# Performance work log

Measured on AMD Instinct MI355X. Metric: run time of the kernel, lower is better.

The kernel has to match this reference:

```python
import jax, jax.numpy as jnp
import numpy as np

B, S, D = 4, 2048, 512
H = 8
DEPTH = D // H  # 64


def setup_inputs() -> dict:
    key = jax.random.key(0)
    ks = jax.random.split(key, 6)
    scale = 1.0 / np.sqrt(D)
    return {
        "x": jax.random.normal(ks[0], (B, S, D), dtype=jnp.float32),
        "y": jax.random.normal(ks[1], (B, S, D), dtype=jnp.float32),
        "W_q": jax.random.normal(ks[2], (D, D), dtype=jnp.float32) * scale,
        "W_k": jax.random.normal(ks[3], (D, D), dtype=jnp.float32) * scale,
        "W_v": jax.random.normal(ks[4], (D, D), dtype=jnp.float32) * scale,
        "W_o": jax.random.normal(ks[5], (D, D), dtype=jnp.float32) * scale,
    }


def _split_heads(t):
    # [B, S, D] -> [B, H, S, DEPTH]
    b, s, _ = t.shape
    return t.reshape(b, s, H, DEPTH).transpose(0, 2, 1, 3)


def reference(x, y, W_q, W_k, W_v, W_o):
    q = _split_heads(x @ W_q) * (DEPTH ** -0.5)   # [B,H,Sq,d]
    k = _split_heads(y @ W_k)                      # [B,H,Sk,d]
    v = _split_heads(y @ W_v)                      # [B,H,Sk,d]
    logits = jnp.einsum("bhqd,bhkd->bhqk", q, k)   # [B,H,Sq,Sk]
    weights = jax.nn.softmax(logits, axis=-1)
    attn = jnp.einsum("bhqk,bhkd->bhqd", weights, v)  # [B,H,Sq,d]
    attn = attn.transpose(0, 2, 1, 3).reshape(x.shape[0], x.shape[1], D)
    return attn @ W_o
```

## Files before the change

### kernel.cpp

```cpp
#include <hip/hip_runtime.h>
#include <hip/hip_bf16.h>
#include <math.h>
#include <stdint.h>

#define NB 4
#define NS 2048
#define ND 512
#define NH 8
#define DEP 64

typedef __attribute__((ext_vector_type(8))) short bf16x8;
typedef __attribute__((ext_vector_type(4))) short bf16x4;
typedef __attribute__((ext_vector_type(4))) float f32x4;
typedef __attribute__((ext_vector_type(16))) float f32x16;

#define QSCALE 0.18033688011112042f

__device__ __forceinline__ short f2b(float f) {
  unsigned u = __float_as_uint(f);
  u += 0x7FFF + ((u >> 16) & 1);
  return (short)(u >> 16);
}
__device__ __forceinline__ unsigned pk2(float a, float b) {
  union { __hip_bfloat162 h; unsigned u; } c;
  c.h = __float22bfloat162_rn(float2{a, b});
  return c.u;
}
__device__ __forceinline__ void dma16(const void* g, void* l) {
  __builtin_amdgcn_global_load_lds(
      (const __attribute__((address_space(1))) void*)g,
      (__attribute__((address_space(3))) void*)l, 16, 0, 0);
}

__global__ __launch_bounds__(256) void prep(
    const float* __restrict__ x, const float* __restrict__ y,
    const float* __restrict__ W0, const float* __restrict__ W1,
    const float* __restrict__ W2, const float* __restrict__ W3,
    short* __restrict__ xb, short* __restrict__ yb, short* __restrict__ T0,
    short* __restrict__ T1, short* __restrict__ T2, short* __restrict__ T3) {
  const int t = threadIdx.x;
  if (blockIdx.y < 2) {
    const float* src = blockIdx.y ? y : x;
    short* dst = blockIdx.y ? yb : xb;
    size_t i = ((size_t)blockIdx.x * 256 + t) * 4;
    float4 v = *(const float4*)(src + i);
    bf16x4 o;
    o[0] = f2b(v.x); o[1] = f2b(v.y); o[2] = f2b(v.z); o[3] = f2b(v.w);
    *(bf16x4*)(dst + i) = o;
    return;
  }
  const int bx = blockIdx.x;
  if (bx >= 256) return;
  const int wj = bx >> 6, rem = bx & 63;
  const float* W = wj == 0 ? W0 : wj == 1 ? W1 : wj == 2 ? W2 : W3;
  short* T = wj == 0 ? T0 : wj == 1 ? T1 : wj == 2 ? T2 : T3;
  __shared__ float tile[64][65];
  const int k0 = (rem >> 3) * 64, n0 = (rem & 7) * 64;
#pragma unroll
  for (int i = 0; i < 4; ++i) {
    int r = (t >> 4) + i * 16;
    int c = (t & 15) * 4;
    float4 v = *(const float4*)&W[(size_t)(k0 + r) * ND + n0 + c];
    tile[r][c] = v.x; tile[r][c + 1] = v.y;
    tile[r][c + 2] = v.z; tile[r][c + 3] = v.w;
  }
  __syncthreads();
#pragma unroll
  for (int i = 0; i < 4; ++i) {
    int n = (t >> 4) + i * 16;
    int kc = (t & 15) * 4;
    bf16x4 o;
#pragma unroll
    for (int j = 0; j < 4; ++j) o[j] = f2b(tile[kc + j][n]);
    *(bf16x4*)&T[(size_t)(n0 + n) * ND + k0 + kc] = o;
  }
}

__device__ __forceinline__ void gemm128(const short* __restrict__ A,
                                        const short* __restrict__ Bt,
                                        short* __restrict__ Cout, int mode,
                                        float alpha) {
  __shared__ short As[128 * 64];
  __shared__ short Bs[128 * 64];
  const int t = threadIdx.x;
  const int wave = t >> 6, lane = t & 63;
  const int m = lane & 15, quad = lane >> 4;
  const int m0 = blockIdx.y * 128, n0 = blockIdx.x * 128;
  const int mh = (wave >> 1) * 64, nh = (wave & 1) * 64;
  const int r8 = lane >> 3;
  const int c8 = (lane & 7) ^ r8;
  const int mx7 = m & 7;
  f32x4 acc[4][4];
#pragma unroll
  for (int i = 0; i < 4; ++i)
#pragma unroll
    for (int j = 0; j < 4; ++j) acc[i][j] = (f32x4){0.f, 0.f, 0.f, 0.f};

  for (int k0 = 0; k0 < ND; k0 += 64) {
    __syncthreads();
#pragma unroll
    for (int i = 0; i < 4; ++i) {
      int row = i * 32 + wave * 8 + r8;
      dma16(A + (size_t)(m0 + row) * ND + k0 + c8 * 8,
            As + (i * 256 + wave * 64) * 8);
      dma16(Bt + (size_t)(n0 + row) * ND + k0 + c8 * 8,
            Bs + (i * 256 + wave * 64) * 8);
    }
    __syncthreads();
    bf16x8 af[4][2], bf[4][2];
#pragma unroll
    for (int mt = 0; mt < 4; ++mt)
#pragma unroll
      for (int kc = 0; kc < 2; ++kc)
        af[mt][kc] = *(const bf16x8*)(As + (mh + mt * 16 + m) * 64 +
                                      ((kc * 4 + quad) ^ mx7) * 8);
#pragma unroll
    for (int nt = 0; nt < 4; ++nt)
#pragma unroll
      for (int kc = 0; kc < 2; ++kc)
        bf[nt][kc] = *(const bf16x8*)(Bs + (nh + nt * 16 + m) * 64 +
                                      ((kc * 4 + quad) ^ mx7) * 8);
#pragma unroll
    for (int mt = 0; mt < 4; ++mt)
#pragma unroll
      for (int nt = 0; nt < 4; ++nt)
#pragma unroll
        for (int kc = 0; kc < 2; ++kc)
          acc[mt][nt] = __builtin_amdgcn_mfma_f32_16x16x32_bf16(
              af[mt][kc], bf[nt][kc], acc[mt][nt], 0, 0, 0);
  }
  if (mode == 2) {
#pragma unroll
    for (int mt = 0; mt < 4; ++mt)
#pragma unroll
      for (int nt = 0; nt < 4; ++nt) {
        int row0 = m0 + mh + mt * 16 + quad * 4;
        int col = n0 + nh + nt * 16 + m;
        int b_ = row0 >> 11, s_ = row0 & (NS - 1);
        int h_ = col >> 6, d_ = col & (DEP - 1);
        uint2 p;
        p.x = pk2(acc[mt][nt][0] * alpha, acc[mt][nt][1] * alpha);
        p.y = pk2(acc[mt][nt][2] * alpha, acc[mt][nt][3] * alpha);
        *(uint2*)(Cout + (size_t)((b_ * NH + h_) * DEP + d_) * NS + s_) = p;
      }
  } else {
#pragma unroll
    for (int mt = 0; mt < 4; ++mt)
#pragma unroll
      for (int nt = 0; nt < 4; ++nt)
#pragma unroll
        for (int r = 0; r < 4; ++r) {
          int row = m0 + mh + mt * 16 + quad * 4 + r;
          int col = n0 + nh + nt * 16 + m;
          Cout[(size_t)row * ND + col] = f2b(acc[mt][nt][r] * alpha);
        }
  }
}

__global__ __launch_bounds__(256) void qkv_gemm(
    const short* __restrict__ xb, const short* __restrict__ yb,
    const short* __restrict__ Wqt, const short* __restrict__ Wkt,
    const short* __restrict__ Wvt, short* __restrict__ Qb,
    short* __restrict__ Kb, short* __restrict__ Vtb) {
  if (blockIdx.z == 0)
    gemm128(xb, Wqt, Qb, 1, QSCALE);
  else if (blockIdx.z == 1)
    gemm128(yb, Wkt, Kb, 1, 1.0f);
  else
    gemm128(yb, Wvt, Vtb, 2, 1.0f);
}

__global__ __launch_bounds__(256) void out_gemm(const short* __restrict__ A,
                                                const short* __restrict__ Bt,
                                                float* __restrict__ Cout) {
  __shared__ short As[2][128 * 64];
  __shared__ short Bs[2][64 * 64];
  const int t = threadIdx.x;
  const int wave = t >> 6, lane = t & 63;
  const int m = lane & 15, quad = lane >> 4;
  const int m0 = blockIdx.y * 128, n0 = blockIdx.x * 64;
  const int mh = (wave >> 1) * 64, nh = (wave & 1) * 32;
  const int r8 = lane >> 3;
  const int c8 = (lane & 7) ^ r8;
  const int mx7 = m & 7;
  f32x4 acc[4][2];
#pragma unroll
  for (int i = 0; i < 4; ++i)
#pragma unroll
    for (int j = 0; j < 2; ++j) acc[i][j] = (f32x4){0.f, 0.f, 0.f, 0.f};

#pragma unroll
  for (int i = 0; i < 4; ++i)
    dma16(A + (size_t)(m0 + i * 32 + wave * 8 + r8) * ND + c8 * 8,
          As[0] + (i * 256 + wave * 64) * 8);
#pragma unroll
  for (int i = 0; i < 2; ++i)
    dma16(Bt + (size_t)(n0 + i * 32 + wave * 8 + r8) * ND + c8 * 8,
          Bs[0] + (i * 256 + wave * 64) * 8);

  int buf = 0;
  for (int k0 = 0; k0 < ND; k0 += 64, buf ^= 1) {
    __syncthreads();
    if (k0 + 64 < ND) {
#pragma unroll
      for (int i = 0; i < 4; ++i)
        dma16(A + (size_t)(m0 + i * 32 + wave * 8 + r8) * ND + k0 + 64 + c8 * 8,
              As[buf ^ 1] + (i * 256 + wave * 64) * 8);
#pragma unroll
      for (int i = 0; i < 2; ++i)
        dma16(Bt + (size_t)(n0 + i * 32 + wave * 8 + r8) * ND + k0 + 64 +
                  c8 * 8,
              Bs[buf ^ 1] + (i * 256 + wave * 64) * 8);
    }
    bf16x8 af[4][2], bf[2][2];
#pragma unroll
    for (int mt = 0; mt < 4; ++mt)
#pragma unroll
      for (int kc = 0; kc < 2; ++kc)
        af[mt][kc] = *(const bf16x8*)(As[buf] + (mh + mt * 16 + m) * 64 +
                                      ((kc * 4 + quad) ^ mx7) * 8);
#pragma unroll
    for (int nt = 0; nt < 2; ++nt)
#pragma unroll
      for (int kc = 0; kc < 2; ++kc)
        bf[nt][kc] = *(const bf16x8*)(Bs[buf] + (nh + nt * 16 + m) * 64 +
                                      ((kc * 4 + quad) ^ mx7) * 8);
#pragma unroll
    for (int mt = 0; mt < 4; ++mt)
#pragma unroll
      for (int nt = 0; nt < 2; ++nt)
#pragma unroll
        for (int kc = 0; kc < 2; ++kc)
          acc[mt][nt] = __builtin_amdgcn_mfma_f32_16x16x32_bf16(
              af[mt][kc], bf[nt][kc], acc[mt][nt], 0, 0, 0);
  }
#pragma unroll
  for (int mt = 0; mt < 4; ++mt)
#pragma unroll
    for (int nt = 0; nt < 2; ++nt)
#pragma unroll
      for (int r = 0; r < 4; ++r) {
        int row = m0 + mh + mt * 16 + quad * 4 + r;
        int col = n0 + nh + nt * 16 + m;
        Cout[(size_t)row * ND + col] = acc[mt][nt][r];
      }
}

__global__ __launch_bounds__(256) void attn_mfma(const short* __restrict__ Qb,
                                                 const short* __restrict__ Kb,
                                                 const short* __restrict__ Vtb,
                                                 short* __restrict__ Ob) {
  __shared__ short Ks[2][64 * 64];
  __shared__ short Vts[2][64 * 64];
  const int t = threadIdx.x;
  const int wave = t >> 6, lane = t & 63;
  const int l31 = lane & 31, hi = lane >> 5;
  const int sw = lane & 7;
  const int bh = blockIdx.y, b = bh >> 3, h = bh & 7;
  const int q0 = blockIdx.x * 128 + wave * 32;
  const size_t rowb = (size_t)b * NS;
  const short* Vtbase = Vtb + (size_t)(bh * DEP) * NS;
  const int r8 = lane >> 3;
  const int c8 = (lane & 7) ^ r8;

  bf16x8 qf[4];
#pragma unroll
  for (int dc = 0; dc < 4; ++dc)
    qf[dc] = *(const bf16x8*)(Qb + (rowb + q0 + l31) * ND + h * DEP + dc * 16 +
                              hi * 8);

  float l_ = 0.0f;
  f32x16 Ot[2];
#pragma unroll
  for (int dt = 0; dt < 2; ++dt)
#pragma unroll
    for (int i = 0; i < 16; ++i) Ot[dt][i] = 0.f;

#pragma unroll
  for (int i = 0; i < 2; ++i) {
    int row = i * 32 + wave * 8 + r8;
    dma16(Kb + (rowb + row) * ND + h * DEP + c8 * 8,
          Ks[0] + (i * 256 + wave * 64) * 8);
    dma16(Vtbase + (size_t)row * NS + c8 * 8,
          Vts[0] + (i * 256 + wave * 64) * 8);
  }

  int buf = 0;
  for (int kv0 = 0; kv0 < NS; kv0 += 64, buf ^= 1) {
    __syncthreads();
    if (kv0 + 64 < NS) {
#pragma unroll
      for (int i = 0; i < 2; ++i) {
        int row = i * 32 + wave * 8 + r8;
        dma16(Kb + (rowb + kv0 + 64 + row) * ND + h * DEP + c8 * 8,
              Ks[buf ^ 1] + (i * 256 + wave * 64) * 8);
        dma16(Vtbase + (size_t)row * NS + kv0 + 64 + c8 * 8,
              Vts[buf ^ 1] + (i * 256 + wave * 64) * 8);
      }
    }

    f32x16 St[2];
#pragma unroll
    for (int kt = 0; kt < 2; ++kt)
#pragma unroll
      for (int i = 0; i < 16; ++i) St[kt][i] = 0.f;
#pragma unroll
    for (int kt = 0; kt < 2; ++kt)
#pragma unroll
      for (int dc = 0; dc < 4; ++dc) {
        bf16x8 kf = *(const bf16x8*)(&Ks[buf][(kt * 32 + l31) * 64 +
                                              ((dc * 2 + hi) ^ sw) * 8]);
        St[kt] = __builtin_amdgcn_mfma_f32_32x32x16_bf16(kf, qf[dc], St[kt],
                                                         0, 0, 0);
      }

    bf16x8 pf[4];
    float rs = 0.f;
#pragma unroll
    for (int s = 0; s < 4; ++s) {
      const int kt = s >> 1, base = (s & 1) * 8;
      float E[8];
#pragma unroll
      for (int j = 0; j < 8; ++j) {
        E[j] = __builtin_amdgcn_exp2f(St[kt][base + j]);
        rs += E[j];
      }
      unsigned A0 = pk2(E[0], E[1]), A1 = pk2(E[2], E[3]);
      unsigned A2 = pk2(E[4], E[5]), A3 = pk2(E[6], E[7]);
      auto r02 =
          __builtin_amdgcn_permlane32_swap((int)A0, (int)A2, false, false);
      auto r13 =
          __builtin_amdgcn_permlane32_swap((int)A1, (int)A3, false, false);
      union { bf16x8 v; int u[4]; } pu;
      pu.u[0] = r02[0]; pu.u[1] = r13[0]; pu.u[2] = r02[1]; pu.u[3] = r13[1];
      pf[s] = pu.v;
    }
    l_ += rs;

#pragma unroll
    for (int dt = 0; dt < 2; ++dt)
#pragma unroll
      for (int s = 0; s < 4; ++s) {
        bf16x8 vf = *(const bf16x8*)(&Vts[buf][(dt * 32 + l31) * 64 +
                                               ((s * 2 + hi) ^ sw) * 8]);
        Ot[dt] = __builtin_amdgcn_mfma_f32_32x32x16_bf16(vf, pf[s], Ot[dt],
                                                         0, 0, 0);
      }
  }

  l_ += __shfl_xor(l_, 32, 64);
  float linv = 1.0f / l_;
  size_t row = rowb + q0 + l31;
#pragma unroll
  for (int dt = 0; dt < 2; ++dt)
#pragma unroll
    for (int g = 0; g < 4; ++g) {
      uint2 pk;
      pk.x = pk2(Ot[dt][g * 4 + 0] * linv, Ot[dt][g * 4 + 1] * linv);
      pk.y = pk2(Ot[dt][g * 4 + 2] * linv, Ot[dt][g * 4 + 3] * linv);
      *(uint2*)(Ob + row * ND + h * DEP + dt * 32 + g * 8 + hi * 4) = pk;
    }
}

extern "C" void kernel_launch(void* const* d_in, const int* in_sizes, int n_in,
                              void* d_out, int out_size, void* d_ws,
                              size_t ws_size, hipStream_t stream) {
  const float* x = (const float*)d_in[0];
  const float* y = (const float*)d_in[1];
  const float* Wq = (const float*)d_in[2];
  const float* Wk = (const float*)d_in[3];
  const float* Wv = (const float*)d_in[4];
  const float* Wo = (const float*)d_in[5];
  float* out = (float*)d_out;

  const size_t mat = (size_t)NB * NS * ND;
  const size_t wsz = (size_t)ND * ND;
  short* xb = (short*)d_ws;
  short* yb = xb + mat;
  short* Wqt = yb + mat;
  short* Wkt = Wqt + wsz;
  short* Wvt = Wkt + wsz;
  short* Wot = Wvt + wsz;
  short* Qb = Wot + wsz;
  short* Kb = Qb + mat;
  short* Vtb = Kb + mat;
  short* attnb = xb;

  prep<<<dim3(mat / 1024, 3), 256, 0, stream>>>(x, y, Wq, Wk, Wv, Wo, xb, yb,
                                                Wqt, Wkt, Wvt, Wot);
  qkv_gemm<<<dim3(ND / 128, (NB * NS) / 128, 3), 256, 0, stream>>>(
      xb, yb, Wqt, Wkt, Wvt, Qb, Kb, Vtb);
  attn_mfma<<<dim3(NS / 128, NB * NH), 256, 0, stream>>>(Qb, Kb, Vtb, attnb);
  out_gemm<<<dim3(ND / 64, (NB * NS) / 128), 256, 0, stream>>>(attnb, Wot,
                                                               out);
}
```

Before: 190.1 us.

## Split attention KV range across two wave groups and merge partials in LDS

The attention kernel now launches 512 threads per block. Two groups of four waves each process half of the key/value sequence for the same 128 queries. The second group writes its unnormalized output and row sums to shared memory, and the first group adds them in, normalizes, and stores the result. This doubles the waves available per block to hide latency, since the grid has only 512 blocks. The cost is double the LDS footprint, an extra merge step with barriers, and more register pressure under the launch-bounds hint. It also makes a small change to the first QK MFMA, which now starts from a zero accumulator, and to the row-sum reduction order.

Result: faster. 184.3 us (-3.1%).

```diff
diff --git a/kernel.cpp b/kernel.cpp
--- a/kernel.cpp
+++ b/kernel.cpp
@@ -8,6 +8,7 @@
 #define ND 512
 #define NH 8
 #define DEP 64
+#define KVHALF (NS / 2)
 
 typedef __attribute__((ext_vector_type(8))) short bf16x8;
 typedef __attribute__((ext_vector_type(4))) short bf16x4;
@@ -246,18 +247,19 @@
       }
 }
 
-__global__ __launch_bounds__(256) void attn_mfma(const short* __restrict__ Qb,
-                                                 const short* __restrict__ Kb,
-                                                 const short* __restrict__ Vtb,
-                                                 short* __restrict__ Ob) {
-  __shared__ short Ks[2][64 * 64];
-  __shared__ short Vts[2][64 * 64];
+__global__ __launch_bounds__(512, 4) void attn_mfma(
+    const short* __restrict__ Qb, const short* __restrict__ Kb,
+    const short* __restrict__ Vtb, short* __restrict__ Ob) {
+  __shared__ short Ks[2][2][64 * 64];
+  __shared__ short Vts[2][2][64 * 64];
   const int t = threadIdx.x;
   const int wave = t >> 6, lane = t & 63;
+  const int zh = wave >> 2, wl = wave & 3;
   const int l31 = lane & 31, hi = lane >> 5;
   const int sw = lane & 7;
   const int bh = blockIdx.y, b = bh >> 3, h = bh & 7;
-  const int q0 = blockIdx.x * 128 + wave * 32;
+  const int q0 = blockIdx.x * 128 + wl * 32;
+  const int kvb = zh * KVHALF;
   const size_t rowb = (size_t)b * NS;
   const short* Vtbase = Vtb + (size_t)(bh * DEP) * NS;
   const int r8 = lane >> 3;
@@ -269,6 +271,10 @@
     qf[dc] = *(const bf16x8*)(Qb + (rowb + q0 + l31) * ND + h * DEP + dc * 16 +
                               hi * 8);
 
+  f32x16 kzero;
+#pragma unroll
+  for (int i = 0; i < 16; ++i) kzero[i] = 0.f;
+
   float l_ = 0.0f;
   f32x16 Ot[2];
 #pragma unroll
@@ -278,41 +284,42 @@
 
 #pragma unroll
   for (int i = 0; i < 2; ++i) {
-    int row = i * 32 + wave * 8 + r8;
-    dma16(Kb + (rowb + row) * ND + h * DEP + c8 * 8,
-          Ks[0] + (i * 256 + wave * 64) * 8);
-    dma16(Vtbase + (size_t)row * NS + c8 * 8,
-          Vts[0] + (i * 256 + wave * 64) * 8);
+    int row = i * 32 + wl * 8 + r8;
+    dma16(Kb + (rowb + kvb + row) * ND + h * DEP + c8 * 8,
+          &Ks[zh][0][(i * 256 + wl * 64) * 8]);
+    dma16(Vtbase + (size_t)row * NS + kvb + c8 * 8,
+          &Vts[zh][0][(i * 256 + wl * 64) * 8]);
   }
 
   int buf = 0;
-  for (int kv0 = 0; kv0 < NS; kv0 += 64, buf ^= 1) {
+  for (int kv0 = 0; kv0 < KVHALF; kv0 += 64, buf ^= 1) {
     __syncthreads();
-    if (kv0 + 64 < NS) {
+    if (kv0 + 64 < KVHALF) {
 #pragma unroll
       for (int i = 0; i < 2; ++i) {
-        int row = i * 32 + wave * 8 + r8;
-        dma16(Kb + (rowb + kv0 + 64 + row) * ND + h * DEP + c8 * 8,
-              Ks[buf ^ 1] + (i * 256 + wave * 64) * 8);
-        dma16(Vtbase + (size_t)row * NS + kv0 + 64 + c8 * 8,
-              Vts[buf ^ 1] + (i * 256 + wave * 64) * 8);
+        int row = i * 32 + wl * 8 + r8;
+        dma16(Kb + (rowb + kvb + kv0 + 64 + row) * ND + h * DEP + c8 * 8,
+              &Ks[zh][buf ^ 1][(i * 256 + wl * 64) * 8]);
+        dma16(Vtbase + (size_t)row * NS + kvb + kv0 + 64 + c8 * 8,
+              &Vts[zh][buf ^ 1][(i * 256 + wl * 64) * 8]);
       }
     }
 
     f32x16 St[2];
 #pragma unroll
-    for (int kt = 0; kt < 2; ++kt)
-#pragma unroll
-      for (int i = 0; i < 16; ++i) St[kt][i] = 0.f;
-#pragma unroll
-    for (int kt = 0; kt < 2; ++kt)
-#pragma unroll
-      for (int dc = 0; dc < 4; ++dc) {
-        bf16x8 kf = *(const bf16x8*)(&Ks[buf][(kt * 32 + l31) * 64 +
-                                              ((dc * 2 + hi) ^ sw) * 8]);
+    for (int kt = 0; kt < 2; ++kt) {
+      bf16x8 kf0 = *(const bf16x8*)(&Ks[zh][buf][(kt * 32 + l31) * 64 +
+                                                 (hi ^ sw) * 8]);
+      St[kt] = __builtin_amdgcn_mfma_f32_32x32x16_bf16(kf0, qf[0], kzero,
+                                                       0, 0, 0);
+#pragma unroll
+      for (int dc = 1; dc < 4; ++dc) {
+        bf16x8 kf = *(const bf16x8*)(&Ks[zh][buf][(kt * 32 + l31) * 64 +
+                                                  ((dc * 2 + hi) ^ sw) * 8]);
         St[kt] = __builtin_amdgcn_mfma_f32_32x32x16_bf16(kf, qf[dc], St[kt],
                                                          0, 0, 0);
       }
+    }
 
     bf16x8 pf[4];
     float rs = 0.f;
@@ -323,8 +330,8 @@
 #pragma unroll
       for (int j = 0; j < 8; ++j) {
         E[j] = __builtin_amdgcn_exp2f(St[kt][base + j]);
-        rs += E[j];
-      }
+      }
+      rs += ((E[0] + E[1]) + (E[2] + E[3])) + ((E[4] + E[5]) + (E[6] + E[7]));
       unsigned A0 = pk2(E[0], E[1]), A1 = pk2(E[2], E[3]);
       unsigned A2 = pk2(E[4], E[5]), A3 = pk2(E[6], E[7]);
       auto r02 =
@@ -341,25 +348,47 @@
     for (int dt = 0; dt < 2; ++dt)
 #pragma unroll
       for (int s = 0; s < 4; ++s) {
-        bf16x8 vf = *(const bf16x8*)(&Vts[buf][(dt * 32 + l31) * 64 +
-                                               ((s * 2 + hi) ^ sw) * 8]);
+        bf16x8 vf = *(const bf16x8*)(&Vts[zh][buf][(dt * 32 + l31) * 64 +
+                                                   ((s * 2 + hi) ^ sw) * 8]);
         Ot[dt] = __builtin_amdgcn_mfma_f32_32x32x16_bf16(vf, pf[s], Ot[dt],
                                                          0, 0, 0);
       }
   }
 
   l_ += __shfl_xor(l_, 32, 64);
-  float linv = 1.0f / l_;
-  size_t row = rowb + q0 + l31;
-#pragma unroll
-  for (int dt = 0; dt < 2; ++dt)
-#pragma unroll
-    for (int g = 0; g < 4; ++g) {
-      uint2 pk;
-      pk.x = pk2(Ot[dt][g * 4 + 0] * linv, Ot[dt][g * 4 + 1] * linv);
-      pk.y = pk2(Ot[dt][g * 4 + 2] * linv, Ot[dt][g * 4 + 3] * linv);
-      *(uint2*)(Ob + row * ND + h * DEP + dt * 32 + g * 8 + hi * 4) = pk;
-    }
+
+  __syncthreads();
+  float* Ox = (float*)Ks;
+  float* lx = (float*)Vts;
+  if (zh == 1) {
+#pragma unroll
+    for (int dt = 0; dt < 2; ++dt)
+#pragma unroll
+      for (int r = 0; r < 16; ++r) {
+        int d = dt * 32 + (r & 3) + 8 * (r >> 2) + 4 * hi;
+        Ox[(wl * 64 + d) * 32 + l31] = Ot[dt][r];
+      }
+    if (lane < 32) lx[wl * 32 + l31] = l_;
+  }
+  __syncthreads();
+  if (zh == 0) {
+    float linv = 1.0f / (l_ + lx[wl * 32 + l31]);
+    size_t row = rowb + q0 + l31;
+#pragma unroll
+    for (int dt = 0; dt < 2; ++dt)
+#pragma unroll
+      for (int g = 0; g < 4; ++g) {
+        int d0 = dt * 32 + g * 8 + hi * 4;
+        float o[4];
+#pragma unroll
+        for (int j = 0; j < 4; ++j)
+          o[j] = Ot[dt][g * 4 + j] + Ox[(wl * 64 + d0 + j) * 32 + l31];
+        uint2 pk;
+        pk.x = pk2(o[0] * linv, o[1] * linv);
+        pk.y = pk2(o[2] * linv, o[3] * linv);
+        *(uint2*)(Ob + row * ND + h * DEP + d0) = pk;
+      }
+  }
 }
 
 extern "C" void kernel_launch(void* const* d_in, const int* in_sizes, int n_in,
@@ -390,7 +419,7 @@
                                                 Wqt, Wkt, Wvt, Wot);
   qkv_gemm<<<dim3(ND / 128, (NB * NS) / 128, 3), 256, 0, stream>>>(
       xb, yb, Wqt, Wkt, Wvt, Qb, Kb, Vtb);
-  attn_mfma<<<dim3(NS / 128, NB * NH), 256, 0, stream>>>(Qb, Kb, Vtb, attnb);
+  attn_mfma<<<dim3(NS / 128, NB * NH), 512, 0, stream>>>(Qb, Kb, Vtb, attnb);
   out_gemm<<<dim3(ND / 64, (NB * NS) / 128), 256, 0, stream>>>(attnb, Wot,
                                                                out);
 }
```
